# Kernel tuning notes

Measured on AMD Instinct MI355X. Metric: run time of the kernel, lower is better.

The kernel has to match this reference:

```python
import jax, jax.numpy as jnp
import numpy as np
import math

B = 128          # batch
D = 512          # d_model
H = 8            # n_heads
L = 6            # n_layers
S = 200          # max_len (fixed by temporal bias table)
LAT = 256        # style_latent_dim + skill_latent_dim
OUT = 6          # output_dim
DK = D // H
DFF = 4 * D


def _ln(x, g, b):
    # torch LayerNorm, eps=1e-5
    mu = jnp.mean(x, axis=-1, keepdims=True)
    var = jnp.mean((x - mu) ** 2, axis=-1, keepdims=True)
    return (x - mu) / jnp.sqrt(var + 1e-5) * g + b


def _gelu(x):
    # torch nn.GELU default = exact (erf) gelu
    return jax.nn.gelu(x, approximate=False)


def setup_inputs() -> dict:
    key = jax.random.key(0)
    ks = iter(jax.random.split(key, 16))
    n = lambda shape: jax.random.normal(next(ks), shape, jnp.float32) * 0.02
    # deterministic temporal bias: bias[i,j] = -0.1*|i-j|/S, shared across heads
    t = jnp.arange(S, dtype=jnp.float32)
    tb = (-0.1 * jnp.abs(t[:, None] - t[None, :]) / S).astype(jnp.float32)
    temp_bias = jnp.broadcast_to(tb, (1, H, S, S)) + 0.0
    inp = {
        'z_style': jax.random.normal(next(ks), (B, 128), jnp.float32),
        'z_skill': jax.random.normal(next(ks), (B, 128), jnp.float32),
        'W_lat': n((LAT, D * S)), 'b_lat': jnp.zeros((D * S,), jnp.float32),
        'temp_bias': temp_bias,
        'Wq': n((L, D, D)), 'bq': jnp.zeros((L, D), jnp.float32),
        'Wk': n((L, D, D)), 'bk': jnp.zeros((L, D), jnp.float32),
        'Wv': n((L, D, D)), 'bv': jnp.zeros((L, D), jnp.float32),
        'Wo': n((L, D, D)), 'bo': jnp.zeros((L, D), jnp.float32),
        'g1': jnp.ones((L, D), jnp.float32), 'be1': jnp.zeros((L, D), jnp.float32),
        'g2': jnp.ones((L, D), jnp.float32), 'be2': jnp.zeros((L, D), jnp.float32),
        'W1': n((L, D, DFF)), 'bf1': jnp.zeros((L, DFF), jnp.float32),
        'W2': n((L, DFF, D)), 'bf2': jnp.zeros((L, D), jnp.float32),
        'Wp1': n((D, D // 2)), 'bp1': jnp.zeros((D // 2,), jnp.float32),
        'Wp2': n((D // 2, OUT)), 'bp2': jnp.zeros((OUT,), jnp.float32),
        'Ws1': n((LAT, D // 2)), 'bs1': jnp.zeros((D // 2,), jnp.float32),
        'Ws2': n((D // 2, 5)), 'bs2': jnp.zeros((5,), jnp.float32),
    }
    return inp


def reference(z_style, z_skill, W_lat, b_lat, temp_bias, Wq, bq, Wk, bk, Wv, bv,
              Wo, bo, g1, be1, g2, be2, W1, bf1, W2, bf2, Wp1, bp1, Wp2, bp2,
              Ws1, bs1, Ws2, bs2):
    z = jnp.concatenate([z_style, z_skill], axis=1)          # [B, LAT]
    x = _gelu(z @ W_lat + b_lat).reshape(-1, S, D)           # [B, S, D]
    # sinusoidal positional encoding (buffer)
    pos = jnp.arange(S, dtype=jnp.float32)[:, None]
    div = jnp.exp(jnp.arange(0, D, 2, dtype=jnp.float32) * (-math.log(10000.0) / D))
    pe = jnp.zeros((S, D), jnp.float32)
    pe = pe.at[:, 0::2].set(jnp.sin(pos * div)).at[:, 1::2].set(jnp.cos(pos * div))
    x = x + pe[None]
    scale = math.sqrt(DK)
    for l in range(L):
        q = (x @ Wq[l] + bq[l]).reshape(-1, S, H, DK)
        k = (x @ Wk[l] + bk[l]).reshape(-1, S, H, DK)
        v = (x @ Wv[l] + bv[l]).reshape(-1, S, H, DK)
        scores = jnp.einsum('bihd,bjhd->bhij', q, k) / scale + temp_bias  # [B,H,S,S]
        w = jax.nn.softmax(scores, axis=-1)
        ctx = jnp.einsum('bhij,bjhd->bihd', w, v).reshape(-1, S, D)
        attn = ctx @ Wo[l] + bo[l]
        x = _ln(x + attn, g1[l], be1[l])
        ff = _gelu(x @ W1[l] + bf1[l]) @ W2[l] + bf2[l]
        x = _ln(x + ff, g2[l], be2[l])
    trajectory = _gelu(x @ Wp1 + bp1) @ Wp2 + bp2            # [B, S, OUT]
    signatures = _gelu(z @ Ws1 + bs1) @ Ws2 + bs2            # [B, 5]
    return trajectory, signatures
```

## Files before the change

kernel.cpp:

```cpp
#include <hip/hip_runtime.h>
#include <math.h>

#define BATCH 128
#define DMODEL 512
#define NHEAD 8
#define NLAYER 6
#define SEQ 200
#define LATDIM 256
#define OUTDIM 6
#define DFF 2048
#define ROWS (BATCH * SEQ)
#define QKVS 1536
#define VTS 264

typedef unsigned short u16;
typedef __attribute__((ext_vector_type(8))) short bfrag8;
typedef __attribute__((ext_vector_type(4))) float facc4;

__device__ __forceinline__ float gelu_f(float v) {
    const float x = v * 0.70710678118654752f;
    const float ax = fabsf(x);
    const float t = __builtin_amdgcn_rcpf(fmaf(0.3275911f, ax, 1.0f));
    float p = fmaf(1.061405429f, t, -1.453152027f);
    p = fmaf(p, t, 1.421413741f);
    p = fmaf(p, t, -0.284496736f);
    p = fmaf(p, t, 0.254829592f);
    p = p * t;
    const float e = __expf(-ax * ax);
    float er = fmaf(-p, e, 1.0f);
    er = copysignf(er, x);
    return 0.5f * v * (1.0f + er);
}
__device__ __forceinline__ u16 f2bf(float f) {
    unsigned u = __float_as_uint(f);
    u += 0x7fffu + ((u >> 16) & 1u);
    return (u16)(u >> 16);
}
__device__ __forceinline__ void gl_lds16(const u16* g, u16* l) {
    __builtin_amdgcn_global_load_lds(
        (const __attribute__((address_space(1))) void*)(uintptr_t)g,
        (__attribute__((address_space(3))) void*)(uintptr_t)l,
        16, 0, 0);
}

enum { MM_QKV = 0, MM_RESID = 1, MM_GELU_BF16 = 2, MM_GELU_F32 = 3, MM_LAT = 4 };

__global__ __launch_bounds__(256) void mm_kernel(
    const u16* __restrict__ A, const u16* __restrict__ Bt,
    const float* __restrict__ bias, float* __restrict__ Cf, u16* __restrict__ Cb,
    const float* __restrict__ pe, int M, int N, int K, int mode, int gx)
{
    __shared__ __align__(16) u16 As[3 * 4096];
    __shared__ __align__(16) u16 Bs[3 * 4096];
    const int tid = threadIdx.x;

    const unsigned nwg = gridDim.x, cpx = nwg >> 3;
    const unsigned id = blockIdx.x;
    const unsigned swz = (id & 7u) * cpx + (id >> 3);
    const int bx = (int)(swz % (unsigned)gx);
    const int by = (int)(swz / (unsigned)gx);
    const int row0 = by * 128, col0 = bx * 128;

    const int lane = tid & 63, w = tid >> 6;
    const int m_w = (w & 1) << 6, n_w = (w >> 1) << 6;
    const int l16 = lane & 15, quad = lane >> 4;

    const int r0 = tid >> 2;
    const int seg = ((tid & 3) ^ ((tid >> 3) & 3)) << 3;
    const u16* Ag0 = A + (size_t)(row0 + r0) * K + seg;
    const u16* Ag1 = A + (size_t)(row0 + r0 + 64) * K + seg;
    const u16* Bg0 = Bt + (size_t)(col0 + r0) * K + seg;
    const u16* Bg1 = Bt + (size_t)(col0 + r0 + 64) * K + seg;

    const int pos = (quad ^ ((l16 >> 1) & 3)) << 3;

    facc4 acc[4][4] = {};
    const int iters = K >> 5;

    u16* Ald = As + w * 512;
    u16* Bld = Bs + w * 512;
    #pragma unroll
    for (int pf = 0; pf < 3; ++pf) {
        const int ko = pf << 5;
        const int bo = pf << 12;
        gl_lds16(Ag0 + ko, Ald + bo);
        gl_lds16(Ag1 + ko, Ald + bo + 2048);
        gl_lds16(Bg0 + ko, Bld + bo);
        gl_lds16(Bg1 + ko, Bld + bo + 2048);
    }

    int b = 0;
    for (int it = 0; it < iters; ++it) {
        const int ahead = iters - 1 - it;
        if (ahead >= 2)      asm volatile("s_waitcnt vmcnt(8)" ::: "memory");
        else if (ahead == 1) asm volatile("s_waitcnt vmcnt(4)" ::: "memory");
        else                 asm volatile("s_waitcnt vmcnt(0)" ::: "memory");
        __builtin_amdgcn_s_barrier();
        asm volatile("" ::: "memory");

        const u16* Ab = As + (b << 12);
        const u16* Bb = Bs + (b << 12);
        bfrag8 af[4], bf[4];
        #pragma unroll
        for (int i = 0; i < 4; ++i)
            af[i] = *(const bfrag8*)&Ab[(m_w + i * 16 + l16) * 32 + pos];
        #pragma unroll
        for (int j = 0; j < 4; ++j)
            bf[j] = *(const bfrag8*)&Bb[(n_w + j * 16 + l16) * 32 + pos];
        __builtin_amdgcn_s_setprio(1);
        #pragma unroll
        for (int i = 0; i < 4; ++i)
            #pragma unroll
            for (int j = 0; j < 4; ++j)
                acc[i][j] = __builtin_amdgcn_mfma_f32_16x16x32_bf16(
                    af[i], bf[j], acc[i][j], 0, 0, 0);
        __builtin_amdgcn_s_setprio(0);

        __builtin_amdgcn_sched_barrier(0);
        asm volatile("" ::: "memory");
        __builtin_amdgcn_s_barrier();
        asm volatile("" ::: "memory");

        if (it + 3 < iters) {
            const int ko = (it + 3) << 5;
            const int bo = b << 12;
            gl_lds16(Ag0 + ko, Ald + bo);
            gl_lds16(Ag1 + ko, Ald + bo + 2048);
            gl_lds16(Bg0 + ko, Bld + bo);
            gl_lds16(Bg1 + ko, Bld + bo + 2048);
        }
        b = (b == 2) ? 0 : b + 1;
    }

    #pragma unroll
    for (int i = 0; i < 4; ++i) {
        #pragma unroll
        for (int r = 0; r < 4; ++r) {
            const int row = row0 + m_w + i * 16 + quad * 4 + r;
            #pragma unroll
            for (int j = 0; j < 4; ++j) {
                const int col = col0 + n_w + j * 16 + l16;
                float v = acc[i][j][r] + bias[col];
                const size_t idx = (size_t)row * N + col;
                if (mode == MM_QKV) {
                    Cb[idx] = f2bf(v);
                } else if (mode == MM_RESID) {
                    Cf[idx] += v;
                } else if (mode == MM_GELU_BF16) {
                    Cb[idx] = f2bf(gelu_f(v));
                } else if (mode == MM_GELU_F32) {
                    Cf[idx] = gelu_f(v);
                } else {
                    v = gelu_f(v) + pe[col];
                    Cf[idx] = v;
                    Cb[idx] = f2bf(v);
                }
            }
        }
    }
}

__global__ __launch_bounds__(256) void pe_kernel(float* __restrict__ pe)
{
    const int idx = blockIdx.x * 256 + threadIdx.x;
    const int s = idx >> 9, d = idx & 511;
    const float ang = (float)s * expf((float)(d & ~1) * (-9.2103403719761836f / 512.0f));
    pe[idx] = (d & 1) ? cosf(ang) : sinf(ang);
}

__global__ __launch_bounds__(256) void attn_kernel(
    const u16* __restrict__ qkv, const float* __restrict__ tb,
    u16* __restrict__ ctxb)
{
    const int qt = blockIdx.x, h = blockIdx.y, b = blockIdx.z;
    const int tid = threadIdx.x;
    const int w = tid >> 6, lane = tid & 63;
    const int l16 = lane & 15, quad = lane >> 4;

    __shared__ __align__(16) u16 kv[16896];
    __shared__ __align__(16) u16 Ps[4][16][232];

    const size_t rowbase = (size_t)b * SEQ;
    const int q0w = qt * 64 + w * 16;

    for (int g = w; g < 26; g += 4) {
        const int c = g * 64 + lane;
        const int key = c >> 3, seg = c & 7;
        const int krow = key < 200 ? key : 199;
        gl_lds16(qkv + (rowbase + krow) * QKVS + 512 + h * 64 +
                 ((seg ^ (key & 7)) << 3),
                 kv + g * 512);
    }
    int qrow = (int)rowbase + q0w + l16;
    if (qrow > ROWS - 1) qrow = ROWS - 1;
    const u16* qp = qkv + (size_t)qrow * QKVS + h * 64 + quad * 8;
    bfrag8 aq0 = *(const bfrag8*)(qp);
    bfrag8 aq1 = *(const bfrag8*)(qp + 32);
    __syncthreads();

    facc4 sc[13];
    #pragma unroll
    for (int nt = 0; nt < 13; ++nt) {
        const int key = nt * 16 + l16, kk = key & 7;
        bfrag8 b0 = *(const bfrag8*)&kv[key * 64 + ((quad ^ kk) << 3)];
        bfrag8 b1 = *(const bfrag8*)&kv[key * 64 + (((4 + quad) ^ kk) << 3)];
        facc4 a = {};
        a = __builtin_amdgcn_mfma_f32_16x16x32_bf16(aq0, b0, a, 0, 0, 0);
        a = __builtin_amdgcn_mfma_f32_16x16x32_bf16(aq1, b1, a, 0, 0, 0);
        sc[nt] = a;
    }
    __syncthreads();

    for (int c = 0; c < 7; ++c) {
        const int key = c * 32 + (tid & 31);
        const int dkb = (tid >> 5) * 8;
        u16 vals[8];
        if (key < 200) {
            *(uint4*)vals = *(const uint4*)(qkv + (rowbase + key) * QKVS +
                                            1024 + h * 64 + dkb);
        } else {
            #pragma unroll
            for (int i = 0; i < 8; ++i) vals[i] = 0;
        }
        #pragma unroll
        for (int i = 0; i < 8; ++i)
            kv[(dkb + i) * VTS + key] = vals[i];
    }

    #pragma unroll
    for (int r = 0; r < 4; ++r) {
        const int i = q0w + quad * 4 + r;
        #pragma unroll
        for (int nt = 0; nt < 13; ++nt) {
            const int j = nt * 16 + l16;
            float s;
            if (j < 200) {
                const float tbv = (i < 200) ? tb[(h * 200 + i) * 200 + j] : 0.f;
                s = sc[nt][r] * 0.125f + tbv;
            } else s = -INFINITY;
            sc[nt][r] = s;
        }
        float m = sc[0][r];
        #pragma unroll
        for (int nt = 1; nt < 13; ++nt) m = fmaxf(m, sc[nt][r]);
        #pragma unroll
        for (int off = 8; off > 0; off >>= 1) m = fmaxf(m, __shfl_xor(m, off, 64));
        float ssum = 0.f;
        #pragma unroll
        for (int nt = 0; nt < 13; ++nt) {
            const float e = __expf(sc[nt][r] - m);
            sc[nt][r] = e; ssum += e;
        }
        #pragma unroll
        for (int off = 8; off > 0; off >>= 1) ssum += __shfl_xor(ssum, off, 64);
        const float inv = 1.0f / ssum;
        #pragma unroll
        for (int nt = 0; nt < 13; ++nt)
            Ps[w][quad * 4 + r][nt * 16 + l16] = f2bf(sc[nt][r] * inv);
        Ps[w][quad * 4 + r][208 + l16] = 0;
    }
    __syncthreads();

    facc4 pacc[4] = {};
    for (int ks = 0; ks < 7; ++ks) {
        bfrag8 ap = *(const bfrag8*)&Ps[w][l16][ks * 32 + quad * 8];
        #pragma unroll
        for (int nt = 0; nt < 4; ++nt) {
            const int dkrow = nt * 16 + l16;
            bfrag8 bv = *(const bfrag8*)&kv[dkrow * VTS + ks * 32 + quad * 8];
            pacc[nt] = __builtin_amdgcn_mfma_f32_16x16x32_bf16(ap, bv, pacc[nt], 0, 0, 0);
        }
    }

    #pragma unroll
    for (int r = 0; r < 4; ++r) {
        const int i = q0w + quad * 4 + r;
        if (i < 200) {
            #pragma unroll
            for (int nt = 0; nt < 4; ++nt)
                ctxb[(rowbase + i) * 512 + h * 64 + nt * 16 + l16] = f2bf(pacc[nt][r]);
        }
    }
}

__global__ __launch_bounds__(256) void tconv_kernel(
    const float* __restrict__ W, u16* __restrict__ O, int K, int N,
    size_t wStride, size_t oStride)
{
    __shared__ u16 T[64][80];
    const float* Wz = W + wStride * blockIdx.z;
    u16* Oz = O + oStride * blockIdx.z;
    const int n0 = blockIdx.x * 64, k0 = blockIdx.y * 64, t = threadIdx.x;
    {
        const int kr = t >> 2, seg = t & 3;
        const float* wp = Wz + (size_t)(k0 + kr) * N + n0 + seg * 16;
        alignas(16) u16 tmp[16];
        #pragma unroll
        for (int q = 0; q < 4; ++q) {
            float4 f = ((const float4*)wp)[q];
            tmp[q * 4 + 0] = f2bf(f.x); tmp[q * 4 + 1] = f2bf(f.y);
            tmp[q * 4 + 2] = f2bf(f.z); tmp[q * 4 + 3] = f2bf(f.w);
        }
        *(uint4*)&T[kr][seg * 16]     = *(uint4*)&tmp[0];
        *(uint4*)&T[kr][seg * 16 + 8] = *(uint4*)&tmp[8];
    }
    __syncthreads();
    {
        const int n = t >> 2, kseg = t & 3;
        alignas(16) u16 o[16];
        #pragma unroll
        for (int i = 0; i < 16; ++i) o[i] = T[kseg * 16 + i][n];
        uint4* op = (uint4*)(Oz + (size_t)(n0 + n) * K + k0 + kseg * 16);
        op[0] = *(uint4*)&o[0];
        op[1] = *(uint4*)&o[8];
    }
}

__global__ __launch_bounds__(256) void tconv4_kernel(
    const float* __restrict__ Wq, const float* __restrict__ Wk,
    const float* __restrict__ Wv, const float* __restrict__ Wo,
    u16* __restrict__ Out)
{
    __shared__ u16 T[64][80];
    const int z = blockIdx.z, layer = z >> 2, m = z & 3;
    const float* W = (m == 0 ? Wq : m == 1 ? Wk : m == 2 ? Wv : Wo)
                     + (size_t)layer * 262144;
    u16* O = Out + (size_t)z * 262144;
    const int n0 = blockIdx.x * 64, k0 = blockIdx.y * 64, t = threadIdx.x;
    {
        const int kr = t >> 2, seg = t & 3;
        const float* wp = W + (size_t)(k0 + kr) * 512 + n0 + seg * 16;
        alignas(16) u16 tmp[16];
        #pragma unroll
        for (int q = 0; q < 4; ++q) {
            float4 f = ((const float4*)wp)[q];
            tmp[q * 4 + 0] = f2bf(f.x); tmp[q * 4 + 1] = f2bf(f.y);
            tmp[q * 4 + 2] = f2bf(f.z); tmp[q * 4 + 3] = f2bf(f.w);
        }
        *(uint4*)&T[kr][seg * 16]     = *(uint4*)&tmp[0];
        *(uint4*)&T[kr][seg * 16 + 8] = *(uint4*)&tmp[8];
    }
    __syncthreads();
    {
        const int n = t >> 2, kseg = t & 3;
        alignas(16) u16 o[16];
        #pragma unroll
        for (int i = 0; i < 16; ++i) o[i] = T[kseg * 16 + i][n];
        uint4* op = (uint4*)(O + (size_t)(n0 + n) * 512 + k0 + kseg * 16);
        op[0] = *(uint4*)&o[0];
        op[1] = *(uint4*)&o[8];
    }
}

__global__ __launch_bounds__(256) void bqkv_kernel(
    const float* __restrict__ bq, const float* __restrict__ bk,
    const float* __restrict__ bv, float* __restrict__ o)
{
    const int l = blockIdx.x, t = threadIdx.x;
    for (int c = t; c < 1536; c += 256) {
        float v = (c < 512) ? bq[l * 512 + c]
                : (c < 1024) ? bk[l * 512 + c - 512]
                             : bv[l * 512 + c - 1024];
        o[l * 1536 + c] = v;
    }
}

__global__ __launch_bounds__(256) void ln_kernel(
    float* __restrict__ x, const float* __restrict__ g,
    const float* __restrict__ bb, u16* __restrict__ xb)
{
    const int w = threadIdx.x >> 6, lane = threadIdx.x & 63;
    const size_t row = (size_t)blockIdx.x * 4 + w;
    float* xr = x + row * DMODEL;
    u16* xbr = xb + row * DMODEL;
    const int c = lane * 8;
    float4 a = *(const float4*)(xr + c);
    float4 b = *(const float4*)(xr + c + 4);
    float s = a.x + a.y + a.z + a.w + b.x + b.y + b.z + b.w;
    #pragma unroll
    for (int off = 32; off > 0; off >>= 1) s += __shfl_xor(s, off, 64);
    const float mu = s * (1.0f / 512.0f);
    a.x -= mu; a.y -= mu; a.z -= mu; a.w -= mu;
    b.x -= mu; b.y -= mu; b.z -= mu; b.w -= mu;
    float v = a.x * a.x + a.y * a.y + a.z * a.z + a.w * a.w
            + b.x * b.x + b.y * b.y + b.z * b.z + b.w * b.w;
    #pragma unroll
    for (int off = 32; off > 0; off >>= 1) v += __shfl_xor(v, off, 64);
    const float rstd = rsqrtf(v * (1.0f / 512.0f) + 1e-5f);
    float4 g0 = *(const float4*)(g + c), g1 = *(const float4*)(g + c + 4);
    float4 b0 = *(const float4*)(bb + c), b1 = *(const float4*)(bb + c + 4);
    float4 o0, o1;
    o0.x = a.x * rstd * g0.x + b0.x; o0.y = a.y * rstd * g0.y + b0.y;
    o0.z = a.z * rstd * g0.z + b0.z; o0.w = a.w * rstd * g0.w + b0.w;
    o1.x = b.x * rstd * g1.x + b1.x; o1.y = b.y * rstd * g1.y + b1.y;
    o1.z = b.z * rstd * g1.z + b1.z; o1.w = b.w * rstd * g1.w + b1.w;
    *(float4*)(xr + c) = o0;
    *(float4*)(xr + c + 4) = o1;
    alignas(16) u16 ob[8] = { f2bf(o0.x), f2bf(o0.y), f2bf(o0.z), f2bf(o0.w),
                              f2bf(o1.x), f2bf(o1.y), f2bf(o1.z), f2bf(o1.w) };
    *(uint4*)(xbr + c) = *(uint4*)ob;
}

__global__ __launch_bounds__(256) void concat_z_kernel(
    const float* __restrict__ zs, const float* __restrict__ zk, u16* __restrict__ z)
{
    const int b = blockIdx.x, t = threadIdx.x;
    z[b * 256 + t] = f2bf((t < 128) ? zs[b * 128 + t] : zk[b * 128 + t - 128]);
}

__global__ __launch_bounds__(64) void traj_head_kernel(
    const float* __restrict__ t1, const float* __restrict__ Wp2,
    const float* __restrict__ bp2, float* __restrict__ out)
{
    const int r = blockIdx.x, t = threadIdx.x;
    __shared__ float red[6][64];
    float p[6] = {};
    const float* tr = t1 + (size_t)r * 256;
    for (int kk = t; kk < 256; kk += 64) {
        float tv = tr[kk];
        #pragma unroll
        for (int c = 0; c < 6; ++c) p[c] = fmaf(tv, Wp2[kk * 6 + c], p[c]);
    }
    #pragma unroll
    for (int c = 0; c < 6; ++c) red[c][t] = p[c];
    __syncthreads();
    if (t < 6) {
        float a = 0.f;
        for (int j = 0; j < 64; ++j) a += red[t][j];
        out[(size_t)r * 6 + t] = a + bp2[t];
    }
}

__global__ __launch_bounds__(256) void sig_head_kernel(
    const float* __restrict__ zs, const float* __restrict__ zk,
    const float* __restrict__ Ws1, const float* __restrict__ bs1,
    const float* __restrict__ Ws2, const float* __restrict__ bs2,
    float* __restrict__ out)
{
    const int b = blockIdx.x, t = threadIdx.x;
    __shared__ float zrow[256];
    __shared__ float h1[256];
    zrow[t] = (t < 128) ? zs[b * 128 + t] : zk[b * 128 + t - 128];
    __syncthreads();
    float acc = bs1[t];
    for (int kk = 0; kk < 256; ++kk) acc = fmaf(zrow[kk], Ws1[kk * 256 + t], acc);
    h1[t] = gelu_f(acc);
    __syncthreads();
    if (t < 5) {
        float a = bs2[t];
        for (int kk = 0; kk < 256; ++kk) a = fmaf(h1[kk], Ws2[kk * 5 + t], a);
        out[b * 5 + t] = a;
    }
}

extern "C" void kernel_launch(void* const* d_in, const int* in_sizes, int n_in,
                              void* d_out, int out_size, void* d_ws, size_t ws_size,
                              hipStream_t stream) {
    const float* z_style   = (const float*)d_in[0];
    const float* z_skill   = (const float*)d_in[1];
    const float* W_lat     = (const float*)d_in[2];
    const float* b_lat     = (const float*)d_in[3];
    const float* temp_bias = (const float*)d_in[4];
    const float* Wq  = (const float*)d_in[5];
    const float* bq  = (const float*)d_in[6];
    const float* Wk  = (const float*)d_in[7];
    const float* bk  = (const float*)d_in[8];
    const float* Wv  = (const float*)d_in[9];
    const float* bv  = (const float*)d_in[10];
    const float* Wo  = (const float*)d_in[11];
    const float* bo  = (const float*)d_in[12];
    const float* g1  = (const float*)d_in[13];
    const float* be1 = (const float*)d_in[14];
    const float* g2  = (const float*)d_in[15];
    const float* be2 = (const float*)d_in[16];
    const float* W1  = (const float*)d_in[17];
    const float* bf1 = (const float*)d_in[18];
    const float* W2  = (const float*)d_in[19];
    const float* bf2 = (const float*)d_in[20];
    const float* Wp1 = (const float*)d_in[21];
    const float* bp1 = (const float*)d_in[22];
    const float* Wp2 = (const float*)d_in[23];
    const float* bp2 = (const float*)d_in[24];
    const float* Ws1 = (const float*)d_in[25];
    const float* bs1 = (const float*)d_in[26];
    const float* Ws2 = (const float*)d_in[27];
    const float* bs2 = (const float*)d_in[28];
    float* out = (float*)d_out;

    char* Wb = (char*)d_ws;
    float* x     = (float*)(Wb + 0);
    u16*  xb     = (u16*)(Wb + 52428800);
    u16*  qkv    = (u16*)(Wb + 78643200);
    u16*  cx     = (u16*)(Wb + 157286400);
    u16*  ff1b   = (u16*)(Wb + 78643200);
    u16*  wlatT  = (u16*)(Wb + 78643200);
    float* t1    = (float*)(Wb + 157286400);
    u16*  qkvoT  = (u16*)(Wb + 183500800);
    u16*  w1T    = (u16*)(Wb + 196083712);
    u16*  w2T    = (u16*)(Wb + 208666624);
    u16*  wp1T   = (u16*)(Wb + 221249536);
    float* bqkv  = (float*)(Wb + 221511680);
    u16*  zbb    = (u16*)(Wb + 221548544);
    float* pe    = (float*)(Wb + 221614080);

    tconv4_kernel<<<dim3(8, 8, 24), 256, 0, stream>>>(Wq, Wk, Wv, Wo, qkvoT);
    tconv_kernel<<<dim3(32, 8, 6), 256, 0, stream>>>(W1, w1T, DMODEL, DFF,
                                                     (size_t)DMODEL * DFF, (size_t)DMODEL * DFF);
    tconv_kernel<<<dim3(8, 32, 6), 256, 0, stream>>>(W2, w2T, DFF, DMODEL,
                                                     (size_t)DMODEL * DFF, (size_t)DMODEL * DFF);
    tconv_kernel<<<dim3(1600, 4, 1), 256, 0, stream>>>(W_lat, wlatT, LATDIM, DMODEL * SEQ, 0, 0);
    tconv_kernel<<<dim3(4, 8, 1), 256, 0, stream>>>(Wp1, wp1T, DMODEL, 256, 0, 0);
    bqkv_kernel<<<NLAYER, 256, 0, stream>>>(bq, bk, bv, bqkv);
    concat_z_kernel<<<BATCH, 256, 0, stream>>>(z_style, z_skill, zbb);
    pe_kernel<<<400, 256, 0, stream>>>(pe);

    mm_kernel<<<dim3(800), 256, 0, stream>>>(
        zbb, wlatT, b_lat, x, xb, pe, BATCH, DMODEL * SEQ, LATDIM, MM_LAT, 800);

    for (int l = 0; l < NLAYER; ++l) {
        mm_kernel<<<dim3(12 * 200), 256, 0, stream>>>(
            xb, qkvoT + (size_t)l * 4 * 262144, bqkv + l * 1536, nullptr, qkv, pe,
            ROWS, QKVS, DMODEL, MM_QKV, 12);
        attn_kernel<<<dim3(4, NHEAD, BATCH), 256, 0, stream>>>(qkv, temp_bias, cx);
        mm_kernel<<<dim3(4 * 200), 256, 0, stream>>>(
            cx, qkvoT + (size_t)(l * 4 + 3) * 262144, bo + l * DMODEL, x, nullptr, pe,
            ROWS, DMODEL, DMODEL, MM_RESID, 4);
        ln_kernel<<<ROWS / 4, 256, 0, stream>>>(x, g1 + l * DMODEL, be1 + l * DMODEL, xb);
        mm_kernel<<<dim3(16 * 200), 256, 0, stream>>>(
            xb, w1T + (size_t)l * DMODEL * DFF, bf1 + l * DFF, nullptr, ff1b, pe,
            ROWS, DFF, DMODEL, MM_GELU_BF16, 16);
        mm_kernel<<<dim3(4 * 200), 256, 0, stream>>>(
            ff1b, w2T + (size_t)l * DMODEL * DFF, bf2 + l * DMODEL, x, nullptr, pe,
            ROWS, DMODEL, DFF, MM_RESID, 4);
        ln_kernel<<<ROWS / 4, 256, 0, stream>>>(x, g2 + l * DMODEL, be2 + l * DMODEL, xb);
    }

    mm_kernel<<<dim3(2 * 200), 256, 0, stream>>>(
        xb, wp1T, bp1, t1, nullptr, pe, ROWS, 256, DMODEL, MM_GELU_F32, 2);
    traj_head_kernel<<<ROWS, 64, 0, stream>>>(t1, Wp2, bp2, out);
    sig_head_kernel<<<BATCH, 256, 0, stream>>>(z_style, z_skill, Ws1, bs1, Ws2, bs2,
                                               out + (size_t)ROWS * OUTDIM);
}
```

Measured before the change: 3.185 ms.

## Add 256x128-tile 512-thread GEMM with triple-buffered LDS for QKV and FFN1

```diff
diff --git a/kernel.cpp b/kernel.cpp
--- a/kernel.cpp
+++ b/kernel.cpp
@@ -155,6 +155,105 @@
                     Cf[idx] = v;
                     Cb[idx] = f2bf(v);
                 }
+            }
+        }
+    }
+}
+
+__global__ __launch_bounds__(512) void mm256_kernel(
+    const u16* __restrict__ A, const u16* __restrict__ Bt,
+    const float* __restrict__ bias, u16* __restrict__ Cb,
+    int N, int K, int mode, int gx)
+{
+    __shared__ __align__(16) u16 As[3 * 8192];
+    __shared__ __align__(16) u16 Bs[3 * 4096];
+    const int tid = threadIdx.x;
+
+    const unsigned nwg = gridDim.x, cpx = nwg >> 3;
+    const unsigned id = blockIdx.x;
+    const unsigned swz = (id & 7u) * cpx + (id >> 3);
+    const int bx = (int)(swz % (unsigned)gx);
+    const int by = (int)(swz / (unsigned)gx);
+    const int row0 = by * 256, col0 = bx * 128;
+
+    const int lane = tid & 63, w = tid >> 6;
+    const int m_w = (w & 3) << 6, n_w = (w >> 2) << 6;
+    const int l16 = lane & 15, quad = lane >> 4;
+
+    const int r0 = tid >> 2;
+    const int seg = ((tid & 3) ^ ((tid >> 3) & 3)) << 3;
+    const u16* Ag0 = A + (size_t)(row0 + r0) * K + seg;
+    const u16* Ag1 = A + (size_t)(row0 + r0 + 128) * K + seg;
+    const u16* Bg0 = Bt + (size_t)(col0 + r0) * K + seg;
+
+    const int pos = (quad ^ ((l16 >> 1) & 3)) << 3;
+
+    facc4 acc[4][4] = {};
+    const int iters = K >> 5;
+
+    u16* Ald = As + w * 512;
+    u16* Bld = Bs + w * 512;
+    #pragma unroll
+    for (int pf = 0; pf < 3; ++pf) {
+        const int ko = pf << 5;
+        gl_lds16(Ag0 + ko, Ald + pf * 8192);
+        gl_lds16(Ag1 + ko, Ald + pf * 8192 + 4096);
+        gl_lds16(Bg0 + ko, Bld + pf * 4096);
+    }
+
+    int b = 0;
+    for (int it = 0; it < iters; ++it) {
+        const int ahead = iters - 1 - it;
+        if (ahead >= 2)      asm volatile("s_waitcnt vmcnt(6)" ::: "memory");
+        else if (ahead == 1) asm volatile("s_waitcnt vmcnt(3)" ::: "memory");
+        else                 asm volatile("s_waitcnt vmcnt(0)" ::: "memory");
+        __builtin_amdgcn_s_barrier();
+        asm volatile("" ::: "memory");
+
+        const u16* Ab = As + b * 8192;
+        const u16* Bb = Bs + b * 4096;
+        bfrag8 af[4], bf[4];
+        #pragma unroll
+        for (int i = 0; i < 4; ++i)
+            af[i] = *(const bfrag8*)&Ab[(m_w + i * 16 + l16) * 32 + pos];
+        #pragma unroll
+        for (int j = 0; j < 4; ++j)
+            bf[j] = *(const bfrag8*)&Bb[(n_w + j * 16 + l16) * 32 + pos];
+        __builtin_amdgcn_s_setprio(1);
+        #pragma unroll
+        for (int i = 0; i < 4; ++i)
+            #pragma unroll
+            for (int j = 0; j < 4; ++j)
+                acc[i][j] = __builtin_amdgcn_mfma_f32_16x16x32_bf16(
+                    af[i], bf[j], acc[i][j], 0, 0, 0);
+        __builtin_amdgcn_s_setprio(0);
+
+        __builtin_amdgcn_sched_barrier(0);
+        asm volatile("" ::: "memory");
+        __builtin_amdgcn_s_barrier();
+        asm volatile("" ::: "memory");
+
+        if (it + 3 < iters) {
+            const int ko = (it + 3) << 5;
+            gl_lds16(Ag0 + ko, Ald + b * 8192);
+            gl_lds16(Ag1 + ko, Ald + b * 8192 + 4096);
+            gl_lds16(Bg0 + ko, Bld + b * 4096);
+        }
+        b = (b == 2) ? 0 : b + 1;
+    }
+
+    #pragma unroll
+    for (int i = 0; i < 4; ++i) {
+        #pragma unroll
+        for (int r = 0; r < 4; ++r) {
+            const int row = row0 + m_w + i * 16 + quad * 4 + r;
+            #pragma unroll
+            for (int j = 0; j < 4; ++j) {
+                const int col = col0 + n_w + j * 16 + l16;
+                float v = acc[i][j][r] + bias[col];
+                const size_t idx = (size_t)row * N + col;
+                if (mode == MM_QKV) Cb[idx] = f2bf(v);
+                else                Cb[idx] = f2bf(gelu_f(v));
             }
         }
     }
@@ -518,17 +617,17 @@
         zbb, wlatT, b_lat, x, xb, pe, BATCH, DMODEL * SEQ, LATDIM, MM_LAT, 800);
 
     for (int l = 0; l < NLAYER; ++l) {
-        mm_kernel<<<dim3(12 * 200), 256, 0, stream>>>(
-            xb, qkvoT + (size_t)l * 4 * 262144, bqkv + l * 1536, nullptr, qkv, pe,
-            ROWS, QKVS, DMODEL, MM_QKV, 12);
+        mm256_kernel<<<dim3(12 * 100), 512, 0, stream>>>(
+            xb, qkvoT + (size_t)l * 4 * 262144, bqkv + l * 1536, qkv,
+            QKVS, DMODEL, MM_QKV, 12);
         attn_kernel<<<dim3(4, NHEAD, BATCH), 256, 0, stream>>>(qkv, temp_bias, cx);
         mm_kernel<<<dim3(4 * 200), 256, 0, stream>>>(
             cx, qkvoT + (size_t)(l * 4 + 3) * 262144, bo + l * DMODEL, x, nullptr, pe,
             ROWS, DMODEL, DMODEL, MM_RESID, 4);
         ln_kernel<<<ROWS / 4, 256, 0, stream>>>(x, g1 + l * DMODEL, be1 + l * DMODEL, xb);
-        mm_kernel<<<dim3(16 * 200), 256, 0, stream>>>(
-            xb, w1T + (size_t)l * DMODEL * DFF, bf1 + l * DFF, nullptr, ff1b, pe,
-            ROWS, DFF, DMODEL, MM_GELU_BF16, 16);
+        mm256_kernel<<<dim3(16 * 100), 512, 0, stream>>>(
+            xb, w1T + (size_t)l * DMODEL * DFF, bf1 + l * DFF, ff1b,
+            DFF, DMODEL, MM_GELU_BF16, 16);
         mm_kernel<<<dim3(4 * 200), 256, 0, stream>>>(
             ff1b, w2T + (size_t)l * DMODEL * DFF, bf2 + l * DMODEL, x, nullptr, pe,
             ROWS, DMODEL, DFF, MM_RESID, 4);
```

Result: faster. 3.113 ms (-2.3%).
